# Performance work log

Hardware: AMD Instinct MI355X
Metric: run time of the kernel (lower is better)

Reference implementation:

```python
import jax, jax.numpy as jnp
import numpy as np

D = 2            # stalk dimension d
FD = 3           # final_d = d + 1 (add_lp=True, add_hp=False)
HID = 32         # hidden_channels
N_NODES = 50000
E0 = 200000      # undirected edges; directed edge list has 2*E0 entries (second half reversed)
IN_CH = 128
OUT_CH = 32
N_LAYERS = 2
PSIZE = D * (D + 1) // 2  # cayley param size per edge


def _spectral_normalize(W, iters=20):
    # torch spectral_norm: power iteration with detached u, v; sigma = u^T W v
    u = jnp.full((W.shape[0],), 1.0 / np.sqrt(W.shape[0]), W.dtype)
    def body(_, u):
        v = W.T @ u
        v = v / (jnp.linalg.norm(v) + 1e-12)
        u2 = W @ v
        return u2 / (jnp.linalg.norm(u2) + 1e-12)
    u = jax.lax.fori_loop(0, iters, body, u)
    u = jax.lax.stop_gradient(u)
    v = jax.lax.stop_gradient(W.T @ u)
    v = v / (jnp.linalg.norm(v) + 1e-12)
    return W / (u @ W @ v)


def _cayley(p):
    # p: [E, PSIZE] lower-tri params -> skew A -> orthogonal Q = (I - A)^{-1}(I + A)
    E = p.shape[0]
    r, c = jnp.tril_indices(D)
    M = jnp.zeros((E, D, D), p.dtype).at[:, r, c].set(p)
    A = M - jnp.swapaxes(M, 1, 2)
    I = jnp.eye(D, dtype=p.dtype)
    return jnp.linalg.solve(I[None] - A, I[None] + A)


def setup_inputs() -> dict:
    key = jax.random.key(0)
    ks = jax.random.split(key, 8)
    src = jax.random.randint(ks[0], (E0,), 0, N_NODES)
    dst = jax.random.randint(ks[1], (E0,), 0, N_NODES)
    # symmetric directed edge list; edge j and edge j+E0 are reverses of each other
    edge_index = jnp.concatenate([jnp.stack([src, dst]), jnp.stack([dst, src])], axis=1)
    x = jax.random.normal(ks[2], (N_NODES, IN_CH), jnp.float32)
    s = 0.02
    W1 = jax.random.normal(ks[3], (FD * HID, IN_CH), jnp.float32) * s
    b1 = jnp.zeros((FD * HID,), jnp.float32)
    W2 = jax.random.normal(ks[4], (OUT_CH, FD * HID), jnp.float32) * s
    b2 = jnp.zeros((OUT_CH,), jnp.float32)
    W_left = jnp.tile(jnp.eye(FD, dtype=jnp.float32)[None], (N_LAYERS, 1, 1))  # init eye per torch
    W_right = jax.random.normal(ks[5], (N_LAYERS, HID, HID), jnp.float32) / np.sqrt(HID)
    eps = jnp.zeros((N_LAYERS, FD, 1), jnp.float32)
    W_sheaf = jax.random.normal(ks[6], (N_LAYERS, PSIZE, 2 * FD * HID), jnp.float32) * s
    W_wt = jax.random.normal(ks[7], (N_LAYERS, 1, 2 * FD * HID), jnp.float32) * s
    return {"x": x, "edge_index": edge_index, "W1": W1, "b1": b1, "W2": W2, "b2": b2,
            "W_left": W_left, "W_right": W_right, "eps": eps, "W_sheaf": W_sheaf, "W_wt": W_wt}


def reference(x, edge_index, W1, b1, W2, b2, W_left, W_right, eps, W_sheaf, W_wt):
    N = x.shape[0]
    row, col = edge_index[0], edge_index[1]
    e0 = row.shape[0] // 2
    rev = jnp.concatenate([jnp.arange(e0) + e0, jnp.arange(e0)])  # reverse-edge index
    # lin1 + ELU (dropouts = 0 in eval)
    h = jax.nn.elu(x @ W1.T + b1)                 # [N, FD*HID]
    xc = h.reshape(N * FD, HID)                   # [N*FD, HID]
    x0 = xc
    for layer in range(N_LAYERS):
        # --- sheaf learner + edge weight learner (gather endpoint features) ---
        xn = xc.reshape(N, FD * HID)
        cat = jnp.concatenate([xn[row], xn[col]], axis=-1)   # [2*E0, 2*FD*HID]
        p = jnp.tanh(cat @ W_sheaf[layer].T)                 # sheaf map params [2*E0, PSIZE]
        wdir = jax.nn.sigmoid(cat @ W_wt[layer].T)[:, 0]
        w = wdir * wdir[rev]                                 # symmetric edge weight
        # --- normalized connection (bundle) Laplacian ---
        Q = _cayley(p)                                       # per-edge orthogonal maps
        T = jnp.einsum('eij,eik->ejk', Q, Q[rev])            # transport F_u^T F_v
        w2 = w * w
        deg = jax.ops.segment_sum(w2, row, num_segments=N)
        dinv = jnp.where(deg > 0, jax.lax.rsqrt(jnp.maximum(deg, 1e-30)), 0.0)
        cnorm = w2 * dinv[row] * dinv[col]                   # [2*E0]
        # --- left / right weights (spectral-normalized) ---
        Wl = _spectral_normalize(W_left[layer])
        Wr = _spectral_normalize(W_right[layer])
        y = xc.reshape(N, FD, HID)
        y = jnp.einsum('ef,nfh->neh', Wl, y)                 # mix stalk dims
        y = jnp.einsum('neh,ch->nec', y, Wr)                 # mix channels
        # --- apply block-sparse Laplacian: Lx[u] = x[u] - sum_e c_e B_e x[v] ---
        yv = y[col]                                          # gather  [2*E0, FD, HID]
        tv = jnp.concatenate([jnp.einsum('eij,ejh->eih', T, yv[:, :D]), yv[:, D:]], axis=1)
        agg = jax.ops.segment_sum(cnorm[:, None, None] * tv, row, num_segments=N)
        diag = jnp.where(deg > 0, 1.0, 0.0)[:, None, None]
        z = jax.nn.elu((diag * y - agg).reshape(N * FD, HID))
        # --- epsilon-gated residual ---
        coeff = jnp.tile(1.0 + jnp.tanh(eps[layer]), (N, 1))  # [N*FD, 1]
        x0 = coeff * x0 - z
        xc = x0
    return xc.reshape(N, FD * HID) @ W2.T + b2
```

## Files before the change

kernel.cpp:

```cpp
#include <hip/hip_runtime.h>

#define NN 50000
#define E0 200000
#define E2 400000
#define NGROUPS ((NN + 7) / 8)
#define NCHUNK  ((NN + 255) / 256)
#define NTILES  ((NN + 63) / 64)
#define EB      ((E2 + 255) / 256)

typedef __attribute__((ext_vector_type(8))) short short8;
typedef __attribute__((ext_vector_type(4))) float f32x4;

__device__ __forceinline__ float eluf(float x) { return x > 0.0f ? x : expm1f(x); }
__device__ __forceinline__ float fsig(float x) { return 1.0f / (1.0f + __expf(-x)); }
__device__ __forceinline__ float ftanh(float x) {
    float e = __expf(-2.0f * x);
    return (1.0f - e) / (1.0f + e);
}
__device__ __forceinline__ unsigned rne_bf16(float x) {
    unsigned u = __float_as_uint(x);
    return (u + 0x7fffu + ((u >> 16) & 1u)) >> 16;
}

__global__ __launch_bounds__(256) void k_setup(const float* __restrict__ Wl_in, const float* __restrict__ Wr_in,
                                               float* __restrict__ Wl_out, float* __restrict__ Wr_out,
                                               int* __restrict__ cnt, int* __restrict__ fill,
                                               float* __restrict__ deg0, int* __restrict__ gtotal) {
    __shared__ float W[32 * 33];
    __shared__ float us[32], vs[32], tmp[32];
    __shared__ float scal;
    int t = threadIdx.x;
    if (blockIdx.x < 2) {
        int l = blockIdx.x;
        for (int i = t; i < 1024; i += 256) W[(i >> 5) * 33 + (i & 31)] = Wr_in[l * 1024 + i];
        if (t < 32) us[t] = 0.17677669529663688f;
        __syncthreads();
        for (int it = 0; it < 20; ++it) {
            if (t < 32) { float a = 0; for (int r = 0; r < 32; ++r) a = fmaf(W[r * 33 + t], us[r], a); tmp[t] = a; }
            __syncthreads();
            if (t == 0) { float s = 0; for (int c = 0; c < 32; ++c) s += tmp[c] * tmp[c]; scal = 1.0f / (sqrtf(s) + 1e-12f); }
            __syncthreads();
            if (t < 32) vs[t] = tmp[t] * scal;
            __syncthreads();
            if (t < 32) { float a = 0; for (int c = 0; c < 32; ++c) a = fmaf(W[t * 33 + c], vs[c], a); tmp[t] = a; }
            __syncthreads();
            if (t == 0) { float s = 0; for (int r = 0; r < 32; ++r) s += tmp[r] * tmp[r]; scal = 1.0f / (sqrtf(s) + 1e-12f); }
            __syncthreads();
            if (t < 32) us[t] = tmp[t] * scal;
            __syncthreads();
        }
        if (t < 32) { float a = 0; for (int r = 0; r < 32; ++r) a = fmaf(W[r * 33 + t], us[r], a); tmp[t] = a; }
        __syncthreads();
        if (t == 0) {
            float s = 0; for (int c = 0; c < 32; ++c) s += tmp[c] * tmp[c];
            scal = (sqrtf(s) + 1e-12f) / s;
        }
        __syncthreads();
        for (int i = t; i < 1024; i += 256) Wr_out[l * 1024 + i] = W[(i >> 5) * 33 + (i & 31)] * scal;
        if (t == 0) {
            float M[9];
            for (int i = 0; i < 9; ++i) M[i] = Wl_in[l * 9 + i];
            float u[3] = {0.5773502691896258f, 0.5773502691896258f, 0.5773502691896258f};
            float v[3], u2[3];
            for (int it = 0; it < 20; ++it) {
                float s = 0;
                for (int c = 0; c < 3; ++c) { v[c] = M[c] * u[0] + M[3 + c] * u[1] + M[6 + c] * u[2]; s += v[c] * v[c]; }
                float inv = 1.0f / (sqrtf(s) + 1e-12f);
                for (int c = 0; c < 3; ++c) v[c] *= inv;
                s = 0;
                for (int r = 0; r < 3; ++r) { u2[r] = M[r * 3] * v[0] + M[r * 3 + 1] * v[1] + M[r * 3 + 2] * v[2]; s += u2[r] * u2[r]; }
                inv = 1.0f / (sqrtf(s) + 1e-12f);
                for (int r = 0; r < 3; ++r) u[r] = u2[r] * inv;
            }
            float s = 0;
            for (int c = 0; c < 3; ++c) { v[c] = M[c] * u[0] + M[3 + c] * u[1] + M[6 + c] * u[2]; s += v[c] * v[c]; }
            float inv = (sqrtf(s) + 1e-12f) / s;
            for (int i = 0; i < 9; ++i) Wl_out[l * 9 + i] = M[i] * inv;
        }
    } else {
        int base = (blockIdx.x - 2) * 256 + t;
        int stride = (gridDim.x - 2) * 256;
        if (blockIdx.x == 2 && t == 0) *gtotal = 0;
        for (int i = base; i < NN; i += stride) { cnt[i] = 0; fill[i] = 0; deg0[i] = 0.0f; }
    }
}

template<int K, int N, int NH, bool ELU, bool HIST>
__global__ __launch_bounds__(256) void k_gemm(const float* __restrict__ X,
                                              const float* __restrict__ W,
                                              const float* __restrict__ bias,
                                              float* __restrict__ out,
                                              const int* __restrict__ row, int* __restrict__ cnt) {
    constexpr int KP = K + 8;
    constexpr int NT = NH / 16;
    constexpr int KS = K / 32;
    constexpr int NHALVES = N / NH;
    __shared__ __align__(16) unsigned short whi[NH * KP];
    __shared__ __align__(16) unsigned short wlo[NH * KP];
    int tid = threadIdx.x;
    if (HIST) {
        for (int e = blockIdx.x * 256 + tid; e < E2; e += gridDim.x * 256)
            atomicAdd(&cnt[row[e]], 1);
    }
    const int ch = blockIdx.x % NHALVES;
    const int tstream = blockIdx.x / NHALVES;
    const int nstreams = gridDim.x / NHALVES;
    for (int i = tid; i < NH * K; i += 256) {
        float v = W[ch * NH * K + i];
        int r = i / K, c = i % K;
        unsigned h = rne_bf16(v);
        whi[r * KP + c] = (unsigned short)h;
        wlo[r * KP + c] = (unsigned short)rne_bf16(v - __uint_as_float(h << 16));
    }
    __syncthreads();
    int wave = tid >> 6, lane = tid & 63;
    int quad = lane >> 4, r16 = lane & 15;
    for (int t = tstream; t < NTILES; t += nstreams) {
        long m = (long)t * 64 + wave * 16 + r16;
        long mc = m < NN ? m : (NN - 1);
        const float* xrow = X + mc * K + quad * 8;
        short8 ah[KS], al[KS];
#pragma unroll
        for (int ks = 0; ks < KS; ++ks) {
            const float4* xp = (const float4*)(xrow + ks * 32);
            float4 p0 = xp[0], p1 = xp[1];
            float xv[8] = {p0.x, p0.y, p0.z, p0.w, p1.x, p1.y, p1.z, p1.w};
#pragma unroll
            for (int j = 0; j < 8; ++j) {
                unsigned h = rne_bf16(xv[j]);
                ah[ks][j] = (short)h;
                al[ks][j] = (short)rne_bf16(xv[j] - __uint_as_float(h << 16));
            }
        }
        long mbase = (long)t * 64 + wave * 16 + quad * 4;
#pragma unroll
        for (int tt = 0; tt < NT; ++tt) {
            f32x4 acc = (f32x4){0.f, 0.f, 0.f, 0.f};
#pragma unroll
            for (int ks = 0; ks < KS; ++ks) {
                int ro = (tt * 16 + r16) * KP + ks * 32 + quad * 8;
                short8 bh = *(const short8*)&whi[ro];
                short8 bl = *(const short8*)&wlo[ro];
                acc = __builtin_amdgcn_mfma_f32_16x16x32_bf16(ah[ks], bh, acc, 0, 0, 0);
                acc = __builtin_amdgcn_mfma_f32_16x16x32_bf16(al[ks], bh, acc, 0, 0, 0);
                acc = __builtin_amdgcn_mfma_f32_16x16x32_bf16(ah[ks], bl, acc, 0, 0, 0);
            }
            int coln = ch * NH + tt * 16 + r16;
            float b = bias[coln];
#pragma unroll
            for (int rr = 0; rr < 4; ++rr) {
                long mm = mbase + rr;
                if (mm < NN) {
                    float v = acc[rr] + b;
                    if (ELU) v = eluf(v);
                    out[mm * N + coln] = v;
                }
            }
        }
    }
}

__global__ __launch_bounds__(256) void k_scan(const int* __restrict__ cnt, int* __restrict__ start,
                                              int* __restrict__ gtotal) {
    __shared__ int s[256];
    __shared__ int soff;
    int b = blockIdx.x, t = threadIdx.x;
    int i = b * 256 + t;
    int v = (i < NN) ? cnt[i] : 0;
    s[t] = v;
    __syncthreads();
    for (int off = 1; off < 256; off <<= 1) {
        int add = (t >= off) ? s[t - off] : 0;
        __syncthreads();
        s[t] += add;
        __syncthreads();
    }
    if (t == 255) soff = atomicAdd(gtotal, s[255]);
    __syncthreads();
    if (i < NN) start[i] = s[t] - v + soff;
}

__global__ __launch_bounds__(256) void k_filly8(const float* __restrict__ xc,
                                                const float* __restrict__ Wl, const float* __restrict__ Wr,
                                                const float* __restrict__ Wsh, const float* __restrict__ Wwt,
                                                unsigned* __restrict__ yA, unsigned short* __restrict__ yB,
                                                float4* __restrict__ proj,
                                                const int* __restrict__ row, const int* __restrict__ start,
                                                int* __restrict__ fill, int* __restrict__ eslot) {
    int tid = threadIdx.x;
    if (blockIdx.x >= NGROUPS) {
        int e = (blockIdx.x - NGROUPS) * 256 + tid;
        if (e < E2) {
            int u = row[e];
            eslot[e] = start[u] + atomicAdd(&fill[u], 1);
        }
        return;
    }
    __shared__ float wrs[32 * 33];
    __shared__ float wls[9];
    __shared__ float xcs[8][96];
    __shared__ float ws1[192], wt[192];
    int n0 = blockIdx.x * 8;
    for (int i = tid; i < 1024; i += 256) wrs[(i >> 5) * 33 + (i & 31)] = Wr[i];
    if (tid < 9) wls[tid] = Wl[tid];
    if (tid < 192) {
        ws1[tid] = Wsh[192 + tid];
        wt[tid]  = Wwt[tid];
    }
    for (int i = tid; i < 192; i += 256) {
        int nd = i / 24, of = (i % 24) * 4;
        *(float4*)&xcs[nd][of] = *(const float4*)&xc[(n0 + nd) * 96 + of];
    }
    __syncthreads();
    int node = tid >> 5, c = tid & 31;
    int n = n0 + node;
    float a1 = 0, a2 = 0, a3 = 0, a4 = 0;
#pragma unroll
    for (int j = 0; j < 3; ++j) {
        int k = j * 32 + c;
        float xv = xcs[node][k];
        a1 = fmaf(xv, ws1[k], a1);
        a2 = fmaf(xv, ws1[96 + k], a2);
        a3 = fmaf(xv, wt[k], a3);
        a4 = fmaf(xv, wt[96 + k], a4);
    }
#pragma unroll
    for (int off = 16; off; off >>= 1) {
        a1 += __shfl_xor(a1, off);
        a2 += __shfl_xor(a2, off);
        a3 += __shfl_xor(a3, off);
        a4 += __shfl_xor(a4, off);
    }
    if (c == 0) proj[n] = make_float4(a1, a2, a3, a4);
    {
        float t0 = 0, t1 = 0, t2 = 0;
        const float* wr = &wrs[c * 33];
        const float* xr = xcs[node];
#pragma unroll
        for (int h = 0; h < 32; ++h) {
            float w = wr[h];
            t0 = fmaf(xr[h], w, t0);
            t1 = fmaf(xr[32 + h], w, t1);
            t2 = fmaf(xr[64 + h], w, t2);
        }
        float o0 = wls[0] * t0 + wls[1] * t1 + wls[2] * t2;
        float o1 = wls[3] * t0 + wls[4] * t1 + wls[5] * t2;
        float o2 = wls[6] * t0 + wls[7] * t1 + wls[8] * t2;
        yA[n * 32 + c] = rne_bf16(o0) | (rne_bf16(o1) << 16);
        yB[n * 32 + c] = (unsigned short)rne_bf16(o2);
    }
}

__global__ __launch_bounds__(256) void k_coef(const int* __restrict__ row, const int* __restrict__ col,
                                              const int* __restrict__ eslot,
                                              const float4* __restrict__ proj,
                                              uint2* __restrict__ meta, float* __restrict__ deg) {
    int e = blockIdx.x * 256 + threadIdx.x;
    if (e >= E0) return;
    int u = row[e], v = col[e];
    float4 pu = proj[u], pv = proj[v];
    float a_e = ftanh(pu.x + pv.y);
    float a_r = ftanh(pv.x + pu.y);
    float wd_e = fsig(pu.z + pv.w);
    float wd_r = fsig(pv.z + pu.w);
    float w = wd_e * wd_r;
    float w2 = w * w;
    float ie = 1.0f / (1.0f + a_e * a_e), ir = 1.0f / (1.0f + a_r * a_r);
    float ce = (1.0f - a_e * a_e) * ie, se = 2.0f * a_e * ie;
    float cr = (1.0f - a_r * a_r) * ir, sr = 2.0f * a_r * ir;
    float C = ce * cr + se * sr;
    float S = ce * sr - se * cr;
    unsigned cb = rne_bf16(C), sb = rne_bf16(S), wb = rne_bf16(w2);
    meta[eslot[e]]      = make_uint2(cb | (sb << 16), (unsigned)v | (wb << 16));
    meta[eslot[e + E0]] = make_uint2(cb | ((sb ^ 0x8000u) << 16), (unsigned)u | (wb << 16));
    atomicAdd(&deg[u], w2);
    atomicAdd(&deg[v], w2);
}

__device__ __forceinline__ void gather_accum(int s0, int ec, int c,
                                             const uint2* __restrict__ meta,
                                             const float* __restrict__ deg, float du,
                                             const unsigned* __restrict__ yA,
                                             const unsigned short* __restrict__ yB,
                                             float& acc0, float& acc1, float& acc2) {
    for (int bs = 0; bs < ec; bs += 32) {
        int nb2 = min(32, ec - bs);
        float CC = 0, SS = 0, cnl = 0;
        int vj = 0;
        if (c < nb2) {
            uint2 mt = meta[s0 + bs + c];
            vj = (int)(mt.y & 0xffffu);
            float w2 = __uint_as_float(mt.y & 0xffff0000u);
            float Cv = __uint_as_float(mt.x << 16);
            float Sv = __uint_as_float(mt.x & 0xffff0000u);
            float dv = deg[vj];
            float dvi = dv > 0.0f ? rsqrtf(fmaxf(dv, 1e-30f)) : 0.0f;
            cnl = w2 * du * dvi;
            CC = cnl * Cv;
            SS = cnl * Sv;
        }
        int j4 = nb2 & ~3;
        int j = 0;
        for (; j < j4; j += 4) {
#pragma unroll
            for (int jj = 0; jj < 4; ++jj) {
                float Cj = __shfl(CC, j + jj, 32);
                float Sj = __shfl(SS, j + jj, 32);
                float cj = __shfl(cnl, j + jj, 32);
                int v = __shfl(vj, j + jj, 32);
                unsigned ua = yA[v * 32 + c];
                unsigned ub = (unsigned)yB[v * 32 + c];
                float y0 = __uint_as_float(ua << 16);
                float y1 = __uint_as_float(ua & 0xffff0000u);
                float y2 = __uint_as_float(ub << 16);
                acc0 = fmaf(Cj, y0, acc0);
                acc0 = fmaf(-Sj, y1, acc0);
                acc1 = fmaf(Sj, y0, acc1);
                acc1 = fmaf(Cj, y1, acc1);
                acc2 = fmaf(cj, y2, acc2);
            }
        }
        for (; j < nb2; ++j) {
            float Cj = __shfl(CC, j, 32);
            float Sj = __shfl(SS, j, 32);
            float cj = __shfl(cnl, j, 32);
            int v = __shfl(vj, j, 32);
            unsigned ua = yA[v * 32 + c];
            unsigned ub = (unsigned)yB[v * 32 + c];
            float y0 = __uint_as_float(ua << 16);
            float y1 = __uint_as_float(ua & 0xffff0000u);
            float y2 = __uint_as_float(ub << 16);
            acc0 = fmaf(Cj, y0, acc0);
            acc0 = fmaf(-Sj, y1, acc0);
            acc1 = fmaf(Sj, y0, acc1);
            acc1 = fmaf(Cj, y1, acc1);
            acc2 = fmaf(cj, y2, acc2);
        }
    }
}

__global__ __launch_bounds__(256) void k_gatherY(const int* __restrict__ start,
                                                 const int* __restrict__ cnt,
                                                 const uint2* __restrict__ meta,
                                                 const float* __restrict__ deg0,
                                                 const unsigned* __restrict__ yA0,
                                                 const unsigned short* __restrict__ yB0,
                                                 const float* __restrict__ eps,
                                                 float* __restrict__ xc,
                                                 const float* __restrict__ Wl, const float* __restrict__ Wr,
                                                 const float* __restrict__ Wsh, const float* __restrict__ Wwt,
                                                 unsigned* __restrict__ yA1, unsigned short* __restrict__ yB1,
                                                 float4* __restrict__ proj, float* __restrict__ deg1) {
    __shared__ float wrs[32 * 33];
    __shared__ float wls[9];
    __shared__ float xcs[8][96];
    __shared__ float ws1[192], wt[192];
    int tid = threadIdx.x;
    for (int i = tid; i < 1024; i += 256) wrs[(i >> 5) * 33 + (i & 31)] = Wr[i];
    if (tid < 9) wls[tid] = Wl[tid];
    if (tid < 192) {
        ws1[tid] = Wsh[(1 * 3 + 1) * 192 + tid];
        wt[tid]  = Wwt[1 * 192 + tid];
    }
    int node = tid >> 5, c = tid & 31;
    int n = blockIdx.x * 8 + node;
    int s0 = start[n], ec = cnt[n];
    float dn = deg0[n];
    float du = dn > 0.0f ? rsqrtf(fmaxf(dn, 1e-30f)) : 0.0f;
    float acc0 = 0, acc1 = 0, acc2 = 0;
    gather_accum(s0, ec, c, meta, deg0, du, yA0, yB0, acc0, acc1, acc2);
    float diag = dn > 0.0f ? 1.0f : 0.0f;
    unsigned ua = yA0[n * 32 + c];
    unsigned ub = (unsigned)yB0[n * 32 + c];
    float oy0 = __uint_as_float(ua << 16);
    float oy1 = __uint_as_float(ua & 0xffff0000u);
    float oy2 = __uint_as_float(ub << 16);
    float c0 = 1.0f + tanhf(eps[0]);
    float c1 = 1.0f + tanhf(eps[1]);
    float c2 = 1.0f + tanhf(eps[2]);
    int base = n * 96 + c;
    float nx0 = c0 * xc[base]      - eluf(diag * oy0 - acc0);
    float nx1 = c1 * xc[base + 32] - eluf(diag * oy1 - acc1);
    float nx2 = c2 * xc[base + 64] - eluf(diag * oy2 - acc2);
    xc[base] = nx0; xc[base + 32] = nx1; xc[base + 64] = nx2;
    if (c == 0) deg1[n] = 0.0f;
    xcs[node][c] = nx0; xcs[node][32 + c] = nx1; xcs[node][64 + c] = nx2;
    __syncthreads();
    float a1 = nx0 * ws1[c] + nx1 * ws1[32 + c] + nx2 * ws1[64 + c];
    float a2 = nx0 * ws1[96 + c] + nx1 * ws1[128 + c] + nx2 * ws1[160 + c];
    float a3 = nx0 * wt[c] + nx1 * wt[32 + c] + nx2 * wt[64 + c];
    float a4 = nx0 * wt[96 + c] + nx1 * wt[128 + c] + nx2 * wt[160 + c];
#pragma unroll
    for (int off = 16; off; off >>= 1) {
        a1 += __shfl_xor(a1, off);
        a2 += __shfl_xor(a2, off);
        a3 += __shfl_xor(a3, off);
        a4 += __shfl_xor(a4, off);
    }
    if (c == 0) proj[n] = make_float4(a1, a2, a3, a4);
    {
        float t0 = 0, t1 = 0, t2 = 0;
        const float* wr = &wrs[c * 33];
        const float* xr = xcs[node];
#pragma unroll
        for (int h = 0; h < 32; ++h) {
            float w = wr[h];
            t0 = fmaf(xr[h], w, t0);
            t1 = fmaf(xr[32 + h], w, t1);
            t2 = fmaf(xr[64 + h], w, t2);
        }
        float o0 = wls[0] * t0 + wls[1] * t1 + wls[2] * t2;
        float o1 = wls[3] * t0 + wls[4] * t1 + wls[5] * t2;
        float o2 = wls[6] * t0 + wls[7] * t1 + wls[8] * t2;
        yA1[n * 32 + c] = rne_bf16(o0) | (rne_bf16(o1) << 16);
        yB1[n * 32 + c] = (unsigned short)rne_bf16(o2);
    }
}

__global__ __launch_bounds__(256) void k_gather(const int* __restrict__ start,
                                                const int* __restrict__ cnt,
                                                const uint2* __restrict__ meta,
                                                const float* __restrict__ deg,
                                                const unsigned* __restrict__ yA,
                                                const unsigned short* __restrict__ yB,
                                                const float* __restrict__ eps,
                                                int layer, float* __restrict__ xc) {
    int tid = threadIdx.x;
    int node = tid >> 5, c = tid & 31;
    int n = blockIdx.x * 8 + node;
    if (n >= NN) return;
    int s0 = start[n], ec = cnt[n];
    float dn = deg[n];
    float du = dn > 0.0f ? rsqrtf(fmaxf(dn, 1e-30f)) : 0.0f;
    float acc0 = 0, acc1 = 0, acc2 = 0;
    gather_accum(s0, ec, c, meta, deg, du, yA, yB, acc0, acc1, acc2);
    float diag = dn > 0.0f ? 1.0f : 0.0f;
    unsigned ua = yA[n * 32 + c];
    unsigned ub = (unsigned)yB[n * 32 + c];
    float oy0 = __uint_as_float(ua << 16);
    float oy1 = __uint_as_float(ua & 0xffff0000u);
    float oy2 = __uint_as_float(ub << 16);
    float c0 = 1.0f + tanhf(eps[layer * 3 + 0]);
    float c1 = 1.0f + tanhf(eps[layer * 3 + 1]);
    float c2 = 1.0f + tanhf(eps[layer * 3 + 2]);
    int base = n * 96 + c;
    float z0 = eluf(diag * oy0 - acc0);
    float z1 = eluf(diag * oy1 - acc1);
    float z2 = eluf(diag * oy2 - acc2);
    xc[base]      = c0 * xc[base]      - z0;
    xc[base + 32] = c1 * xc[base + 32] - z1;
    xc[base + 64] = c2 * xc[base + 64] - z2;
}

extern "C" void kernel_launch(void* const* d_in, const int* in_sizes, int n_in,
                              void* d_out, int out_size, void* d_ws, size_t ws_size,
                              hipStream_t stream) {
    const float* x     = (const float*)d_in[0];
    const int*   ei    = (const int*)d_in[1];
    const float* W1    = (const float*)d_in[2];
    const float* b1    = (const float*)d_in[3];
    const float* W2    = (const float*)d_in[4];
    const float* b2    = (const float*)d_in[5];
    const float* Wl    = (const float*)d_in[6];
    const float* Wr    = (const float*)d_in[7];
    const float* eps   = (const float*)d_in[8];
    const float* Wsh   = (const float*)d_in[9];
    const float* Wwt   = (const float*)d_in[10];
    float* out = (float*)d_out;
    const int* row = ei;
    const int* col = ei + E2;

    char* pc = (char*)d_ws;
    float* xc     = (float*)pc;          pc += (size_t)NN * 96 * 4;
    uint2* meta   = (uint2*)pc;          pc += (size_t)E2 * 8;
    unsigned* yA0 = (unsigned*)pc;       pc += (size_t)NN * 32 * 4;
    unsigned* yA1 = (unsigned*)pc;       pc += (size_t)NN * 32 * 4;
    unsigned short* yB0 = (unsigned short*)pc; pc += (size_t)NN * 32 * 2;
    unsigned short* yB1 = (unsigned short*)pc; pc += (size_t)NN * 32 * 2;
    pc = (char*)(((size_t)pc + 15) & ~(size_t)15);
    float4* proj  = (float4*)pc;         pc += (size_t)NN * 16;
    float* deg0   = (float*)pc;          pc += (size_t)NN * 4;
    float* deg1   = (float*)pc;          pc += (size_t)NN * 4;
    float* Wl_n   = (float*)pc;          pc += 32 * 4;
    float* Wr_n   = (float*)pc;          pc += 2048 * 4;
    int* cnt      = (int*)pc;            pc += (size_t)NN * 4;
    int* start    = (int*)pc;            pc += (size_t)NN * 4;
    int* fill     = (int*)pc;            pc += (size_t)NN * 4;
    int* eslot    = (int*)pc;            pc += (size_t)E2 * 4;
    int* gtotal   = (int*)pc;            pc += 4;

    k_setup<<<34, 256, 0, stream>>>(Wl, Wr, Wl_n, Wr_n, cnt, fill, deg0, gtotal);
    k_gemm<128, 96, 48, true, true><<<512, 256, 0, stream>>>(x, W1, b1, xc, row, cnt);
    k_scan<<<NCHUNK, 256, 0, stream>>>(cnt, start, gtotal);
    k_filly8<<<NGROUPS + EB, 256, 0, stream>>>(xc, Wl_n, Wr_n, Wsh, Wwt,
                                               yA0, yB0, proj, row, start, fill, eslot);
    k_coef<<<(E0 + 255) / 256, 256, 0, stream>>>(row, col, eslot, proj, meta, deg0);
    k_gatherY<<<NGROUPS, 256, 0, stream>>>(start, cnt, meta, deg0, yA0, yB0, eps, xc,
                                           Wl_n + 9, Wr_n + 1024, Wsh, Wwt, yA1, yB1, proj, deg1);
    k_coef<<<(E0 + 255) / 256, 256, 0, stream>>>(row, col, eslot, proj, meta, deg1);
    k_gather<<<NGROUPS, 256, 0, stream>>>(start, cnt, meta, deg1, yA1, yB1, eps, 1, xc);
    k_gemm<96, 32, 32, false, false><<<512, 256, 0, stream>>>(xc, W2, b2, out, nullptr, nullptr);
}
```

Measured before the change: 321.7 us.

## Use warp-shuffle power iteration in setup and retune grid sizes

The spectral-norm power iteration for the right weight is rewritten to run inside a single 32-lane group. It uses shuffles and xor reductions instead of shared-memory round trips with many block barriers, and the 3x3 left-weight iteration now runs on a separate thread concurrently. The init part of k_setup now launches one block per 256-node chunk instead of a grid-stride loop over 32 blocks. The first GEMM grid is raised to 1024 blocks and the final GEMM to 782, and a barrier in k_gatherY is moved earlier so shared weights are loaded before use. The setup kernel is serial and short, so the main gain would be lower latency on the critical-path launch, plus better occupancy from the GEMM grid changes.

Measured after the change: 318.9 us. About the same (-0.9%).

```diff
diff --git a/kernel.cpp b/kernel.cpp
--- a/kernel.cpp
+++ b/kernel.cpp
@@ -22,67 +22,75 @@
     return (u + 0x7fffu + ((u >> 16) & 1u)) >> 16;
 }
 
+__device__ __forceinline__ void spectral_block(int l, const float* __restrict__ Wl_in,
+                                               const float* __restrict__ Wr_in,
+                                               float* __restrict__ Wl_out, float* __restrict__ Wr_out) {
+    __shared__ float W[32 * 33];
+    __shared__ float sscal;
+    int t = threadIdx.x;
+    for (int i = t; i < 1024; i += 256) W[(i >> 5) * 33 + (i & 31)] = Wr_in[l * 1024 + i];
+    __syncthreads();
+    if (t < 32) {
+        float u = 0.17677669529663688f;
+        for (int it = 0; it < 20; ++it) {
+            float v = 0.f;
+#pragma unroll 8
+            for (int r = 0; r < 32; ++r) v = fmaf(W[r * 33 + t], __shfl(u, r, 32), v);
+            float s = v * v;
+#pragma unroll
+            for (int off = 16; off; off >>= 1) s += __shfl_xor(s, off, 32);
+            v *= 1.0f / (sqrtf(s) + 1e-12f);
+            float u2 = 0.f;
+#pragma unroll 8
+            for (int c = 0; c < 32; ++c) u2 = fmaf(W[t * 33 + c], __shfl(v, c, 32), u2);
+            s = u2 * u2;
+#pragma unroll
+            for (int off = 16; off; off >>= 1) s += __shfl_xor(s, off, 32);
+            u = u2 * (1.0f / (sqrtf(s) + 1e-12f));
+        }
+        float v = 0.f;
+#pragma unroll 8
+        for (int r = 0; r < 32; ++r) v = fmaf(W[r * 33 + t], __shfl(u, r, 32), v);
+        float s = v * v;
+#pragma unroll
+        for (int off = 16; off; off >>= 1) s += __shfl_xor(s, off, 32);
+        if (t == 0) sscal = (sqrtf(s) + 1e-12f) / s;
+    } else if (t == 64) {
+        float M[9];
+        for (int i = 0; i < 9; ++i) M[i] = Wl_in[l * 9 + i];
+        float u[3] = {0.5773502691896258f, 0.5773502691896258f, 0.5773502691896258f};
+        float v[3], u2[3];
+        for (int it = 0; it < 20; ++it) {
+            float s = 0;
+            for (int c = 0; c < 3; ++c) { v[c] = M[c] * u[0] + M[3 + c] * u[1] + M[6 + c] * u[2]; s += v[c] * v[c]; }
+            float inv = 1.0f / (sqrtf(s) + 1e-12f);
+            for (int c = 0; c < 3; ++c) v[c] *= inv;
+            s = 0;
+            for (int r = 0; r < 3; ++r) { u2[r] = M[r * 3] * v[0] + M[r * 3 + 1] * v[1] + M[r * 3 + 2] * v[2]; s += u2[r] * u2[r]; }
+            inv = 1.0f / (sqrtf(s) + 1e-12f);
+            for (int r = 0; r < 3; ++r) u[r] = u2[r] * inv;
+        }
+        float s = 0;
+        for (int c = 0; c < 3; ++c) { v[c] = M[c] * u[0] + M[3 + c] * u[1] + M[6 + c] * u[2]; s += v[c] * v[c]; }
+        float inv = (sqrtf(s) + 1e-12f) / s;
+        for (int i = 0; i < 9; ++i) Wl_out[l * 9 + i] = M[i] * inv;
+    }
+    __syncthreads();
+    float invs = sscal;
+    for (int i = t; i < 1024; i += 256) Wr_out[l * 1024 + i] = W[(i >> 5) * 33 + (i & 31)] * invs;
+}
+
 __global__ __launch_bounds__(256) void k_setup(const float* __restrict__ Wl_in, const float* __restrict__ Wr_in,
                                                float* __restrict__ Wl_out, float* __restrict__ Wr_out,
                                                int* __restrict__ cnt, int* __restrict__ fill,
                                                float* __restrict__ deg0, int* __restrict__ gtotal) {
-    __shared__ float W[32 * 33];
-    __shared__ float us[32], vs[32], tmp[32];
-    __shared__ float scal;
-    int t = threadIdx.x;
     if (blockIdx.x < 2) {
-        int l = blockIdx.x;
-        for (int i = t; i < 1024; i += 256) W[(i >> 5) * 33 + (i & 31)] = Wr_in[l * 1024 + i];
-        if (t < 32) us[t] = 0.17677669529663688f;
-        __syncthreads();
-        for (int it = 0; it < 20; ++it) {
-            if (t < 32) { float a = 0; for (int r = 0; r < 32; ++r) a = fmaf(W[r * 33 + t], us[r], a); tmp[t] = a; }
-            __syncthreads();
-            if (t == 0) { float s = 0; for (int c = 0; c < 32; ++c) s += tmp[c] * tmp[c]; scal = 1.0f / (sqrtf(s) + 1e-12f); }
-            __syncthreads();
-            if (t < 32) vs[t] = tmp[t] * scal;
-            __syncthreads();
-            if (t < 32) { float a = 0; for (int c = 0; c < 32; ++c) a = fmaf(W[t * 33 + c], vs[c], a); tmp[t] = a; }
-            __syncthreads();
-            if (t == 0) { float s = 0; for (int r = 0; r < 32; ++r) s += tmp[r] * tmp[r]; scal = 1.0f / (sqrtf(s) + 1e-12f); }
-            __syncthreads();
-            if (t < 32) us[t] = tmp[t] * scal;
-            __syncthreads();
-        }
-        if (t < 32) { float a = 0; for (int r = 0; r < 32; ++r) a = fmaf(W[r * 33 + t], us[r], a); tmp[t] = a; }
-        __syncthreads();
-        if (t == 0) {
-            float s = 0; for (int c = 0; c < 32; ++c) s += tmp[c] * tmp[c];
-            scal = (sqrtf(s) + 1e-12f) / s;
-        }
-        __syncthreads();
-        for (int i = t; i < 1024; i += 256) Wr_out[l * 1024 + i] = W[(i >> 5) * 33 + (i & 31)] * scal;
-        if (t == 0) {
-            float M[9];
-            for (int i = 0; i < 9; ++i) M[i] = Wl_in[l * 9 + i];
-            float u[3] = {0.5773502691896258f, 0.5773502691896258f, 0.5773502691896258f};
-            float v[3], u2[3];
-            for (int it = 0; it < 20; ++it) {
-                float s = 0;
-                for (int c = 0; c < 3; ++c) { v[c] = M[c] * u[0] + M[3 + c] * u[1] + M[6 + c] * u[2]; s += v[c] * v[c]; }
-                float inv = 1.0f / (sqrtf(s) + 1e-12f);
-                for (int c = 0; c < 3; ++c) v[c] *= inv;
-                s = 0;
-                for (int r = 0; r < 3; ++r) { u2[r] = M[r * 3] * v[0] + M[r * 3 + 1] * v[1] + M[r * 3 + 2] * v[2]; s += u2[r] * u2[r]; }
-                inv = 1.0f / (sqrtf(s) + 1e-12f);
-                for (int r = 0; r < 3; ++r) u[r] = u2[r] * inv;
-            }
-            float s = 0;
-            for (int c = 0; c < 3; ++c) { v[c] = M[c] * u[0] + M[3 + c] * u[1] + M[6 + c] * u[2]; s += v[c] * v[c]; }
-            float inv = (sqrtf(s) + 1e-12f) / s;
-            for (int i = 0; i < 9; ++i) Wl_out[l * 9 + i] = M[i] * inv;
-        }
-    } else {
-        int base = (blockIdx.x - 2) * 256 + t;
-        int stride = (gridDim.x - 2) * 256;
-        if (blockIdx.x == 2 && t == 0) *gtotal = 0;
-        for (int i = base; i < NN; i += stride) { cnt[i] = 0; fill[i] = 0; deg0[i] = 0.0f; }
-    }
+        spectral_block((int)blockIdx.x, Wl_in, Wr_in, Wl_out, Wr_out);
+        return;
+    }
+    int i = (blockIdx.x - 2) * 256 + threadIdx.x;
+    if (i == 0) *gtotal = 0;
+    if (i < NN) { cnt[i] = 0; fill[i] = 0; deg0[i] = 0.0f; }
 }
 
 template<int K, int N, int NH, bool ELU, bool HIST>
@@ -362,6 +370,7 @@
         ws1[tid] = Wsh[(1 * 3 + 1) * 192 + tid];
         wt[tid]  = Wwt[1 * 192 + tid];
     }
+    __syncthreads();
     int node = tid >> 5, c = tid & 31;
     int n = blockIdx.x * 8 + node;
     int s0 = start[n], ec = cnt[n];
@@ -385,7 +394,6 @@
     xc[base] = nx0; xc[base + 32] = nx1; xc[base + 64] = nx2;
     if (c == 0) deg1[n] = 0.0f;
     xcs[node][c] = nx0; xcs[node][32 + c] = nx1; xcs[node][64 + c] = nx2;
-    __syncthreads();
     float a1 = nx0 * ws1[c] + nx1 * ws1[32 + c] + nx2 * ws1[64 + c];
     float a2 = nx0 * ws1[96 + c] + nx1 * ws1[128 + c] + nx2 * ws1[160 + c];
     float a3 = nx0 * wt[c] + nx1 * wt[32 + c] + nx2 * wt[64 + c];
@@ -489,8 +497,8 @@
     int* eslot    = (int*)pc;            pc += (size_t)E2 * 4;
     int* gtotal   = (int*)pc;            pc += 4;
 
-    k_setup<<<34, 256, 0, stream>>>(Wl, Wr, Wl_n, Wr_n, cnt, fill, deg0, gtotal);
-    k_gemm<128, 96, 48, true, true><<<512, 256, 0, stream>>>(x, W1, b1, xc, row, cnt);
+    k_setup<<<NCHUNK + 2, 256, 0, stream>>>(Wl, Wr, Wl_n, Wr_n, cnt, fill, deg0, gtotal);
+    k_gemm<128, 96, 48, true, true><<<1024, 256, 0, stream>>>(x, W1, b1, xc, row, cnt);
     k_scan<<<NCHUNK, 256, 0, stream>>>(cnt, start, gtotal);
     k_filly8<<<NGROUPS + EB, 256, 0, stream>>>(xc, Wl_n, Wr_n, Wsh, Wwt,
                                                yA0, yB0, proj, row, start, fill, eslot);
@@ -499,5 +507,5 @@
                                            Wl_n + 9, Wr_n + 1024, Wsh, Wwt, yA1, yB1, proj, deg1);
     k_coef<<<(E0 + 255) / 256, 256, 0, stream>>>(row, col, eslot, proj, meta, deg1);
     k_gather<<<NGROUPS, 256, 0, stream>>>(start, cnt, meta, deg1, yA1, yB1, eps, 1, xc);
-    k_gemm<96, 32, 32, false, false><<<512, 256, 0, stream>>>(xc, W2, b2, out, nullptr, nullptr);
-}
+    k_gemm<96, 32, 32, false, false><<<782, 256, 0, stream>>>(xc, W2, b2, out, nullptr, nullptr);
+}
```
